# Kernel tuning notes

Hardware: AMD Instinct MI355X
Metric: run time of the kernel (lower is better)

Reference implementation:

```python
import jax, jax.numpy as jnp
import numpy as np


def setup_inputs() -> dict:
    key = jax.random.key(0)
    ks = jax.random.split(key, 6)
    L, B, S, D = 2, 32, 2048, 1024
    dec_hidden = jax.random.normal(ks[0], (L, B, D), dtype=jnp.float32)
    enc_out = jax.random.normal(ks[1], (B, S, D), dtype=jnp.float32)
    mask = jax.random.randint(ks[2], (B, S), 0, 2, dtype=jnp.int32)
    sc = 1.0 / np.sqrt(D)
    W_dec = jax.random.normal(ks[3], (D, D), dtype=jnp.float32) * sc
    W_enc = jax.random.normal(ks[4], (D, D), dtype=jnp.float32) * sc
    w_att = jax.random.normal(ks[5], (D, 1), dtype=jnp.float32) * sc
    return {
        "decoder_hidden": dec_hidden,
        "encoder_outputs": enc_out,
        "mask": mask,
        "W_dec": W_dec,
        "b_dec": jnp.zeros((D,), jnp.float32),
        "W_enc": W_enc,
        "b_enc": jnp.zeros((D,), jnp.float32),
        "w_att": w_att,
        "b_att": jnp.zeros((1,), jnp.float32),
    }


def reference(decoder_hidden, encoder_outputs, mask, W_dec, b_dec, W_enc, b_enc, w_att, b_att):
    # decoder_hidden: [L, B, Dd] -> take last layer, project to enc dim: [B, 1, De]
    dec_proj = decoder_hidden[-1] @ W_dec + b_dec            # [B, De]
    enc_proj = jnp.einsum("bse,ef->bsf", encoder_outputs, W_enc) + b_enc  # [B, S, De]
    energy = jnp.tanh(dec_proj[:, None, :] + enc_proj)        # [B, S, De]
    scores = jnp.einsum("bse,eo->bso", energy, w_att)[..., 0] + b_att[0]  # [B, S]
    scores = jnp.where(mask == 0, jnp.float32(-1e10), scores)
    attn = jax.nn.softmax(scores, axis=1)                     # [B, S]
    context = jnp.einsum("bs,bse->be", attn, encoder_outputs)[:, None, :]  # [B, 1, De]
    return context, attn
```

## Files before the change

kernel.cpp:

```cpp
#include <hip/hip_runtime.h>
#include <hip/hip_bf16.h>

constexpr int LAY = 2;
constexpr int BB  = 32;
constexpr int SS  = 2048;
constexpr int DD  = 1024;

typedef unsigned short u16;
typedef short  short8  __attribute__((ext_vector_type(8)));
typedef u16    u16x8   __attribute__((ext_vector_type(8)));
typedef float  floatx4 __attribute__((ext_vector_type(4)));

__device__ inline float bf2f(u16 u) {
    union { unsigned int i; float f; } v; v.i = ((unsigned int)u) << 16; return v.f;
}
__device__ inline u16 f2bf_rn(float f) {
    union { float f; unsigned int i; } v; v.f = f;
    unsigned int x = v.i;
    return (u16)((x + 0x7FFFu + ((x >> 16) & 1u)) >> 16);
}

__device__ __forceinline__ float fast_tanh(float x) {
    float e = __expf(x + x);
    return 1.0f - 2.0f * __builtin_amdgcn_rcpf(e + 1.0f);
}

__device__ __forceinline__ void gload_lds16(const u16* g, u16* l) {
    __builtin_amdgcn_global_load_lds(
        (const __attribute__((address_space(1))) void*)g,
        (__attribute__((address_space(3))) void*)l, 16, 0, 0);
}

__global__ __launch_bounds__(256) void convert_enc(const float* __restrict__ enc,
                                                   u16* __restrict__ encbf) {
    size_t gid = (size_t)blockIdx.x * 256 + threadIdx.x;
    #pragma unroll 4
    for (int it = 0; it < 16; ++it) {
        size_t i = (it * 524288ull + gid) * 8;
        floatx4 v0 = *reinterpret_cast<const floatx4*>(enc + i);
        floatx4 v1 = *reinterpret_cast<const floatx4*>(enc + i + 4);
        u16x8 r;
        #pragma unroll
        for (int j = 0; j < 4; ++j) { r[j] = f2bf_rn(v0[j]); r[4 + j] = f2bf_rn(v1[j]); }
        *reinterpret_cast<u16x8*>(encbf + i) = r;
    }
}

__global__ __launch_bounds__(256) void transpose_wenc(const float* __restrict__ W,
                                                      u16* __restrict__ wT) {
    int gid = blockIdx.x * 256 + threadIdx.x;
    int n = gid & 1023, c = gid >> 10;
    int k0 = c * 8;
    u16x8 r;
    #pragma unroll
    for (int j = 0; j < 8; ++j) r[j] = f2bf_rn(W[(size_t)(k0 + j) * DD + n]);
    *reinterpret_cast<u16x8*>(&wT[(size_t)n * DD + k0]) = r;
}

__global__ __launch_bounds__(256) void dec_proj_kernel(
    const float* __restrict__ dec_hidden, const float* __restrict__ W_dec,
    const float* __restrict__ b_dec, float* __restrict__ dec_proj) {
    int kc = blockIdx.x, cb = blockIdx.y, b = blockIdx.z, t = threadIdx.x;
    int col = cb * 256 + t;
    const float* h = dec_hidden + (LAY - 1) * BB * DD + b * DD + kc * 256;
    const float* Wp = W_dec + (size_t)kc * 256 * DD + col;
    float a0 = 0.f, a1 = 0.f, a2 = 0.f, a3 = 0.f;
    for (int e = 0; e < 256; e += 4) {
        a0 += h[e + 0] * Wp[(size_t)(e + 0) * DD];
        a1 += h[e + 1] * Wp[(size_t)(e + 1) * DD];
        a2 += h[e + 2] * Wp[(size_t)(e + 2) * DD];
        a3 += h[e + 3] * Wp[(size_t)(e + 3) * DD];
    }
    float v = (a0 + a1) + (a2 + a3);
    if (kc == 0) v += b_dec[col];
    atomicAdd(&dec_proj[b * DD + col], v);
}

__global__ __launch_bounds__(256) void score_gemm_bf(
    const u16* __restrict__ enc,
    const u16* __restrict__ wT,
    const float* __restrict__ dec_proj,
    const float* __restrict__ b_enc, const float* __restrict__ w_att,
    float* __restrict__ scores) {
    __shared__ u16 As[128 * 64];
    __shared__ u16 Bs[128 * 64];

    const int tid  = threadIdx.x;
    const int f    = blockIdx.x;
    const int swz  = ((f & 7) << 9) | (f >> 3);
    const int bm   = swz >> 3;
    const int bn   = swz & 7;
    const int row0 = bm * 128, col0 = bn * 128;
    const int lane = tid & 63, w = tid >> 6;
    const int wm   = w >> 1,  wn = w & 1;
    const int quad = lane >> 4, l16 = lane & 15;

    const int srow = w * 8 + (lane >> 3);
    const int scol = (((lane & 7) ^ (lane >> 3)) * 8);

    floatx4 acc[4][4];
    #pragma unroll
    for (int i = 0; i < 4; ++i)
        #pragma unroll
        for (int j = 0; j < 4; ++j)
            acc[i][j] = (floatx4){0.f, 0.f, 0.f, 0.f};

    for (int kt = 0; kt < DD / 64; ++kt) {
        const int k0 = kt * 64;
        __syncthreads();
        #pragma unroll
        for (int i = 0; i < 4; ++i) {
            gload_lds16(&enc[(size_t)(row0 + i * 32 + srow) * DD + k0 + scol],
                        &As[(i * 32 + w * 8) * 64]);
            gload_lds16(&wT [(size_t)(col0 + i * 32 + srow) * DD + k0 + scol],
                        &Bs[(i * 32 + w * 8) * 64]);
        }
        __syncthreads();
        #pragma unroll
        for (int ks = 0; ks < 2; ++ks) {
            short8 a[4], b[4];
            #pragma unroll
            for (int tm = 0; tm < 4; ++tm) {
                int r = wm * 64 + tm * 16 + l16;
                int kcs = (ks * 4 + quad) ^ (l16 & 7);
                a[tm] = *reinterpret_cast<const short8*>(&As[r * 64 + kcs * 8]);
            }
            #pragma unroll
            for (int tn = 0; tn < 4; ++tn) {
                int r = wn * 64 + tn * 16 + l16;
                int kcs = (ks * 4 + quad) ^ (l16 & 7);
                b[tn] = *reinterpret_cast<const short8*>(&Bs[r * 64 + kcs * 8]);
            }
            #pragma unroll
            for (int tm = 0; tm < 4; ++tm)
                #pragma unroll
                for (int tn = 0; tn < 4; ++tn)
                    acc[tm][tn] = __builtin_amdgcn_mfma_f32_16x16x32_bf16(
                        a[tm], b[tn], acc[tm][tn], 0, 0, 0);
        }
    }

    const int bIdx = row0 / SS;
    const float* dp = dec_proj + bIdx * DD;
    float cvec[4], wvv[4];
    #pragma unroll
    for (int tn = 0; tn < 4; ++tn) {
        int n = col0 + wn * 64 + tn * 16 + l16;
        cvec[tn] = dp[n] + b_enc[n];
        wvv[tn]  = w_att[n];
    }
    #pragma unroll
    for (int tm = 0; tm < 4; ++tm) {
        float rs0 = 0.f, rs1 = 0.f, rs2 = 0.f, rs3 = 0.f;
        #pragma unroll
        for (int tn = 0; tn < 4; ++tn) {
            rs0 += fast_tanh(acc[tm][tn][0] + cvec[tn]) * wvv[tn];
            rs1 += fast_tanh(acc[tm][tn][1] + cvec[tn]) * wvv[tn];
            rs2 += fast_tanh(acc[tm][tn][2] + cvec[tn]) * wvv[tn];
            rs3 += fast_tanh(acc[tm][tn][3] + cvec[tn]) * wvv[tn];
        }
        #pragma unroll
        for (int off = 1; off < 16; off <<= 1) {
            rs0 += __shfl_xor(rs0, off, 64);
            rs1 += __shfl_xor(rs1, off, 64);
            rs2 += __shfl_xor(rs2, off, 64);
            rs3 += __shfl_xor(rs3, off, 64);
        }
        if (l16 == 0) {
            int rbase = row0 + wm * 64 + tm * 16 + quad * 4;
            atomicAdd(&scores[rbase + 0], rs0);
            atomicAdd(&scores[rbase + 1], rs1);
            atomicAdd(&scores[rbase + 2], rs2);
            atomicAdd(&scores[rbase + 3], rs3);
        }
    }
}

__global__ __launch_bounds__(256) void softmax_kernel(
    const float* __restrict__ scores, const int* __restrict__ mask,
    float* __restrict__ attn_out) {
    int b = blockIdx.x, t = threadIdx.x;
    const float* srow = scores + b * SS;
    const int*   mrow = mask + b * SS;
    float vals[8];
    float vmax = -1e30f;
    #pragma unroll
    for (int i = 0; i < 8; ++i) {
        int s = i * 256 + t;
        float v = (mrow[s] == 0) ? -1e10f : srow[s];
        vals[i] = v;
        vmax = fmaxf(vmax, v);
    }
    #pragma unroll
    for (int off = 32; off >= 1; off >>= 1) vmax = fmaxf(vmax, __shfl_xor(vmax, off, 64));
    __shared__ float sm[4];
    if ((t & 63) == 0) sm[t >> 6] = vmax;
    __syncthreads();
    vmax = fmaxf(fmaxf(sm[0], sm[1]), fmaxf(sm[2], sm[3]));
    float sum = 0.f;
    #pragma unroll
    for (int i = 0; i < 8; ++i) { vals[i] = __expf(vals[i] - vmax); sum += vals[i]; }
    #pragma unroll
    for (int off = 32; off >= 1; off >>= 1) sum += __shfl_xor(sum, off, 64);
    __shared__ float ssum[4];
    if ((t & 63) == 0) ssum[t >> 6] = sum;
    __syncthreads();
    sum = ssum[0] + ssum[1] + ssum[2] + ssum[3];
    float inv = 1.f / sum;
    #pragma unroll
    for (int i = 0; i < 8; ++i) attn_out[b * SS + i * 256 + t] = vals[i] * inv;
}

__global__ __launch_bounds__(256) void context_bf(
    const float* __restrict__ attn, const u16* __restrict__ encbf,
    float* __restrict__ ctx) {
    int scb = blockIdx.x;
    int b   = blockIdx.y;
    int t   = threadIdx.x;
    int d   = (t & 127) * 8;
    int sh  = t >> 7;
    const float* ar  = attn + b * SS + scb * 128;
    const u16*  base = encbf + ((size_t)b * SS + scb * 128) * DD + d;
    float a[8];
    #pragma unroll
    for (int j = 0; j < 8; ++j) a[j] = 0.f;
    #pragma unroll 4
    for (int so = 0; so < 128; so += 2) {
        int s = so + sh;
        u16x8 v = *reinterpret_cast<const u16x8*>(base + (size_t)s * DD);
        float w = ar[s];
        #pragma unroll
        for (int j = 0; j < 8; ++j) a[j] += w * bf2f(v[j]);
    }
    #pragma unroll
    for (int j = 0; j < 8; ++j) atomicAdd(&ctx[b * DD + d + j], a[j]);
}

extern "C" void kernel_launch(void* const* d_in, const int* in_sizes, int n_in,
                              void* d_out, int out_size, void* d_ws, size_t ws_size,
                              hipStream_t stream) {
    const float* dec_hidden = (const float*)d_in[0];
    const float* enc        = (const float*)d_in[1];
    const int*   mask       = (const int*)d_in[2];
    const float* W_dec      = (const float*)d_in[3];
    const float* b_dec      = (const float*)d_in[4];
    const float* W_enc      = (const float*)d_in[5];
    const float* b_enc      = (const float*)d_in[6];
    const float* w_att      = (const float*)d_in[7];

    float* out = (float*)d_out;
    float* ws  = (float*)d_ws;
    float* dec_proj = ws;
    float* scores   = ws + 32768;
    u16*   wT       = (u16*)(ws + 98304);
    u16*   encbf    = (u16*)(ws + 622592);
    float* attn     = out + 32768;

    hipMemsetAsync(ws, 0, 98304 * sizeof(float), stream);
    hipMemsetAsync(out, 0, 32768 * sizeof(float), stream);

    convert_enc<<<2048, 256, 0, stream>>>(enc, encbf);
    transpose_wenc<<<512, 256, 0, stream>>>(W_enc, wT);
    dec_proj_kernel<<<dim3(4, 4, 32), 256, 0, stream>>>(dec_hidden, W_dec, b_dec, dec_proj);
    score_gemm_bf<<<4096, 256, 0, stream>>>(encbf, wT, dec_proj, b_enc, w_att, scores);
    softmax_kernel<<<32, 256, 0, stream>>>(scores, mask, attn);
    context_bf<<<dim3(16, 32), 256, 0, stream>>>(attn, encbf, out);
}
```

Measured before the change: 697.8 us.

## Enlarge score GEMM tiles to 256x256 with double-buffered LDS pipelining

The bf16 score GEMM moves from 128x128 tiles with 4 waves to 256x256 tiles with 8 waves, each wave holding an 8x4 MFMA accumulator block. LDS is double-buffered, so the next K-slice loads are issued while MFMAs run on the current buffer, with split A/B staging and s_setprio around the MFMA bursts. The aim is more data reuse per loaded byte and overlap of global-to-LDS copies with compute. In exchange it uses 128KB of LDS per block and more accumulator registers, which caps occupancy, and the grid shrinks to 1024 blocks.

```diff
diff --git a/kernel.cpp b/kernel.cpp
--- a/kernel.cpp
+++ b/kernel.cpp
@@ -76,69 +76,47 @@
     atomicAdd(&dec_proj[b * DD + col], v);
 }
 
-__global__ __launch_bounds__(256) void score_gemm_bf(
+__global__ __launch_bounds__(512, 2) void score_gemm_bf(
     const u16* __restrict__ enc,
     const u16* __restrict__ wT,
     const float* __restrict__ dec_proj,
     const float* __restrict__ b_enc, const float* __restrict__ w_att,
     float* __restrict__ scores) {
-    __shared__ u16 As[128 * 64];
-    __shared__ u16 Bs[128 * 64];
+    __shared__ u16 As[2][256 * 64];
+    __shared__ u16 Bs[2][256 * 64];
 
     const int tid  = threadIdx.x;
     const int f    = blockIdx.x;
-    const int swz  = ((f & 7) << 9) | (f >> 3);
-    const int bm   = swz >> 3;
-    const int bn   = swz & 7;
-    const int row0 = bm * 128, col0 = bn * 128;
+    const int swz  = ((f & 7) << 7) | (f >> 3);
+    const int bm   = swz >> 2;
+    const int bn   = swz & 3;
+    const int row0 = bm * 256, col0 = bn * 256;
     const int lane = tid & 63, w = tid >> 6;
-    const int wm   = w >> 1,  wn = w & 1;
+    const int wm   = w >> 2,  wn = w & 3;
     const int quad = lane >> 4, l16 = lane & 15;
 
     const int srow = w * 8 + (lane >> 3);
     const int scol = (((lane & 7) ^ (lane >> 3)) * 8);
 
-    floatx4 acc[4][4];
-    #pragma unroll
-    for (int i = 0; i < 4; ++i)
+    auto stageA = [&](int buf, int k0) {
+        #pragma unroll
+        for (int i = 0; i < 4; ++i)
+            gload_lds16(&enc[(size_t)(row0 + i * 64 + srow) * DD + k0 + scol],
+                        &As[buf][(i * 64 + w * 8) * 64]);
+    };
+    auto stageB = [&](int buf, int k0) {
+        #pragma unroll
+        for (int i = 0; i < 4; ++i)
+            gload_lds16(&wT[(size_t)(col0 + i * 64 + srow) * DD + k0 + scol],
+                        &Bs[buf][(i * 64 + w * 8) * 64]);
+    };
+
+    floatx4 acc[8][4];
+    #pragma unroll
+    for (int i = 0; i < 8; ++i)
         #pragma unroll
         for (int j = 0; j < 4; ++j)
             acc[i][j] = (floatx4){0.f, 0.f, 0.f, 0.f};
-
-    for (int kt = 0; kt < DD / 64; ++kt) {
-        const int k0 = kt * 64;
-        __syncthreads();
-        #pragma unroll
-        for (int i = 0; i < 4; ++i) {
-            gload_lds16(&enc[(size_t)(row0 + i * 32 + srow) * DD + k0 + scol],
-                        &As[(i * 32 + w * 8) * 64]);
-            gload_lds16(&wT [(size_t)(col0 + i * 32 + srow) * DD + k0 + scol],
-                        &Bs[(i * 32 + w * 8) * 64]);
-        }
-        __syncthreads();
-        #pragma unroll
-        for (int ks = 0; ks < 2; ++ks) {
-            short8 a[4], b[4];
-            #pragma unroll
-            for (int tm = 0; tm < 4; ++tm) {
-                int r = wm * 64 + tm * 16 + l16;
-                int kcs = (ks * 4 + quad) ^ (l16 & 7);
-                a[tm] = *reinterpret_cast<const short8*>(&As[r * 64 + kcs * 8]);
-            }
-            #pragma unroll
-            for (int tn = 0; tn < 4; ++tn) {
-                int r = wn * 64 + tn * 16 + l16;
-                int kcs = (ks * 4 + quad) ^ (l16 & 7);
-                b[tn] = *reinterpret_cast<const short8*>(&Bs[r * 64 + kcs * 8]);
-            }
-            #pragma unroll
-            for (int tm = 0; tm < 4; ++tm)
-                #pragma unroll
-                for (int tn = 0; tn < 4; ++tn)
-                    acc[tm][tn] = __builtin_amdgcn_mfma_f32_16x16x32_bf16(
-                        a[tm], b[tn], acc[tm][tn], 0, 0, 0);
-        }
-    }
 
     const int bIdx = row0 / SS;
     const float* dp = dec_proj + bIdx * DD;
@@ -149,8 +127,54 @@
         cvec[tn] = dp[n] + b_enc[n];
         wvv[tn]  = w_att[n];
     }
-    #pragma unroll
-    for (int tm = 0; tm < 4; ++tm) {
+
+    auto phase = [&](int buf, int ks) {
+        short8 a[8], b[4];
+        const int kcs = (ks * 4 + quad) ^ (l16 & 7);
+        #pragma unroll
+        for (int m = 0; m < 8; ++m) {
+            int r = wm * 128 + m * 16 + l16;
+            a[m] = *reinterpret_cast<const short8*>(&As[buf][r * 64 + kcs * 8]);
+        }
+        #pragma unroll
+        for (int n = 0; n < 4; ++n) {
+            int r = wn * 64 + n * 16 + l16;
+            b[n] = *reinterpret_cast<const short8*>(&Bs[buf][r * 64 + kcs * 8]);
+        }
+        __builtin_amdgcn_s_setprio(1);
+        #pragma unroll
+        for (int m = 0; m < 8; ++m)
+            #pragma unroll
+            for (int n = 0; n < 4; ++n)
+                acc[m][n] = __builtin_amdgcn_mfma_f32_16x16x32_bf16(
+                    a[m], b[n], acc[m][n], 0, 0, 0);
+        __builtin_amdgcn_s_setprio(0);
+    };
+
+    #define MID_BAR  do { __builtin_amdgcn_s_barrier(); \
+                          __builtin_amdgcn_sched_barrier(0); } while (0)
+
+    stageA(0, 0); stageB(0, 0);
+    __syncthreads();
+
+    for (int kt = 0; kt < 16; kt += 2) {
+        if (kt + 1 < 16) stageA(1, (kt + 1) * 64);
+        phase(0, 0);
+        MID_BAR;
+        if (kt + 1 < 16) stageB(1, (kt + 1) * 64);
+        phase(0, 1);
+        __syncthreads();
+        if (kt + 2 < 16) stageA(0, (kt + 2) * 64);
+        phase(1, 0);
+        MID_BAR;
+        if (kt + 2 < 16) stageB(0, (kt + 2) * 64);
+        phase(1, 1);
+        __syncthreads();
+    }
+    #undef MID_BAR
+
+    #pragma unroll
+    for (int tm = 0; tm < 8; ++tm) {
         float rs0 = 0.f, rs1 = 0.f, rs2 = 0.f, rs3 = 0.f;
         #pragma unroll
         for (int tn = 0; tn < 4; ++tn) {
@@ -167,7 +191,7 @@
             rs3 += __shfl_xor(rs3, off, 64);
         }
         if (l16 == 0) {
-            int rbase = row0 + wm * 64 + tm * 16 + quad * 4;
+            int rbase = row0 + wm * 128 + tm * 16 + quad * 4;
             atomicAdd(&scores[rbase + 0], rs0);
             atomicAdd(&scores[rbase + 1], rs1);
             atomicAdd(&scores[rbase + 2], rs2);
@@ -262,7 +286,7 @@
     convert_enc<<<2048, 256, 0, stream>>>(enc, encbf);
     transpose_wenc<<<512, 256, 0, stream>>>(W_enc, wT);
     dec_proj_kernel<<<dim3(4, 4, 32), 256, 0, stream>>>(dec_hidden, W_dec, b_dec, dec_proj);
-    score_gemm_bf<<<4096, 256, 0, stream>>>(encbf, wT, dec_proj, b_enc, w_att, scores);
+    score_gemm_bf<<<1024, 512, 0, stream>>>(encbf, wT, dec_proj, b_enc, w_att, scores);
     softmax_kernel<<<32, 256, 0, stream>>>(scores, mask, attn);
     context_bf<<<dim3(16, 32), 256, 0, stream>>>(attn, encbf, out);
 }
```

New measurement: 665.1 us. -4.7%, faster.

## Retile score GEMM to 64x256 with register-direct W fragments and double-buffered A

Applied to the files above, without the earlier changes.

W_enc is now pre-packed into an MFMA-fragment layout, so the score GEMM reads B fragments straight from global memory into registers instead of staging them through LDS. The A tile shrinks to 64 rows and is double-buffered in LDS, while each block covers 256 output columns with four waves, and occupancy is hinted at 4 blocks per CU. The decoder projection now computes all 32 batch rows per block from shared memory so each weight element is read once, and the context kernel grid is doubled for more parallelism. The trade-off is more global and L2 traffic for B fragments each k-step and more atomics in dec_proj, in exchange for less LDS pressure, one fewer barrier per iteration, and overlap of A loads with compute.

```diff
diff --git a/kernel.cpp b/kernel.cpp
--- a/kernel.cpp
+++ b/kernel.cpp
@@ -47,56 +47,70 @@
 }
 
 __global__ __launch_bounds__(256) void transpose_wenc(const float* __restrict__ W,
-                                                      u16* __restrict__ wT) {
+                                                      u16* __restrict__ wt2) {
     int gid = blockIdx.x * 256 + threadIdx.x;
     int n = gid & 1023, c = gid >> 10;
-    int k0 = c * 8;
     u16x8 r;
     #pragma unroll
-    for (int j = 0; j < 8; ++j) r[j] = f2bf_rn(W[(size_t)(k0 + j) * DD + n]);
-    *reinterpret_cast<u16x8*>(&wT[(size_t)n * DD + k0]) = r;
+    for (int j = 0; j < 8; ++j) r[j] = f2bf_rn(W[(size_t)(c * 8 + j) * DD + n]);
+    *reinterpret_cast<u16x8*>(&wt2[((size_t)c * DD + n) * 8]) = r;
 }
 
 __global__ __launch_bounds__(256) void dec_proj_kernel(
     const float* __restrict__ dec_hidden, const float* __restrict__ W_dec,
     const float* __restrict__ b_dec, float* __restrict__ dec_proj) {
-    int kc = blockIdx.x, cb = blockIdx.y, b = blockIdx.z, t = threadIdx.x;
+    int kc = blockIdx.x, cb = blockIdx.y, t = threadIdx.x;
     int col = cb * 256 + t;
-    const float* h = dec_hidden + (LAY - 1) * BB * DD + b * DD + kc * 256;
-    const float* Wp = W_dec + (size_t)kc * 256 * DD + col;
-    float a0 = 0.f, a1 = 0.f, a2 = 0.f, a3 = 0.f;
-    for (int e = 0; e < 256; e += 4) {
-        a0 += h[e + 0] * Wp[(size_t)(e + 0) * DD];
-        a1 += h[e + 1] * Wp[(size_t)(e + 1) * DD];
-        a2 += h[e + 2] * Wp[(size_t)(e + 2) * DD];
-        a3 += h[e + 3] * Wp[(size_t)(e + 3) * DD];
-    }
-    float v = (a0 + a1) + (a2 + a3);
-    if (kc == 0) v += b_dec[col];
-    atomicAdd(&dec_proj[b * DD + col], v);
-}
-
-__global__ __launch_bounds__(256) void score_gemm_bf(
+    __shared__ float sh[32][64];
+    const float* hbase = dec_hidden + (LAY - 1) * BB * DD + kc * 64;
+    #pragma unroll
+    for (int j = 0; j < 8; ++j) {
+        int idx = t + j * 256;
+        int b = idx >> 6, e = idx & 63;
+        sh[b][e] = hbase[(size_t)b * DD + e];
+    }
+    __syncthreads();
+    float acc[32];
+    #pragma unroll
+    for (int b = 0; b < 32; ++b) acc[b] = 0.f;
+    const float* Wp = W_dec + (size_t)kc * 64 * DD + col;
+    for (int e = 0; e < 64; ++e) {
+        float wv = Wp[(size_t)e * DD];
+        #pragma unroll
+        for (int b = 0; b < 32; ++b) acc[b] += sh[b][e] * wv;
+    }
+    float bd = (kc == 0) ? b_dec[col] : 0.f;
+    #pragma unroll
+    for (int b = 0; b < 32; ++b) atomicAdd(&dec_proj[b * DD + col], acc[b] + bd);
+}
+
+__global__ __launch_bounds__(256, 4) void score_gemm_bf(
     const u16* __restrict__ enc,
-    const u16* __restrict__ wT,
+    const u16* __restrict__ wt2,
     const float* __restrict__ dec_proj,
     const float* __restrict__ b_enc, const float* __restrict__ w_att,
     float* __restrict__ scores) {
-    __shared__ u16 As[128 * 64];
-    __shared__ u16 Bs[128 * 64];
+    __shared__ u16 As[2][64 * 64];
 
     const int tid  = threadIdx.x;
     const int f    = blockIdx.x;
     const int swz  = ((f & 7) << 9) | (f >> 3);
-    const int bm   = swz >> 3;
-    const int bn   = swz & 7;
-    const int row0 = bm * 128, col0 = bn * 128;
+    const int bm   = swz >> 2;
+    const int bn   = swz & 3;
+    const int row0 = bm * 64, col0 = bn * 256;
     const int lane = tid & 63, w = tid >> 6;
-    const int wm   = w >> 1,  wn = w & 1;
     const int quad = lane >> 4, l16 = lane & 15;
 
-    const int srow = w * 8 + (lane >> 3);
+    const int srow = lane >> 3;
     const int scol = (((lane & 7) ^ (lane >> 3)) * 8);
+
+    auto stage = [&](int buf, int kt) {
+        const int k0 = kt * 64;
+        #pragma unroll
+        for (int i = 0; i < 2; ++i)
+            gload_lds16(&enc[(size_t)(row0 + w * 16 + i * 8 + srow) * DD + k0 + scol],
+                        &As[buf][(w * 16 + i * 8) * 64]);
+    };
 
     floatx4 acc[4][4];
     #pragma unroll
@@ -105,39 +119,54 @@
         for (int j = 0; j < 4; ++j)
             acc[i][j] = (floatx4){0.f, 0.f, 0.f, 0.f};
 
-    for (int kt = 0; kt < DD / 64; ++kt) {
-        const int k0 = kt * 64;
+    const u16* bbase = wt2 + ((size_t)quad * DD + col0 + w * 64 + l16) * 8;
+
+    stage(0, 0);
+    __syncthreads();
+
+    int buf = 0;
+    for (int kt = 0; kt < 16; ++kt) {
+        short8 b0[4], b1[4];
+        const u16* bk = bbase + (size_t)kt * 8 * DD * 8;
+        #pragma unroll
+        for (int n = 0; n < 4; ++n)
+            b0[n] = *reinterpret_cast<const short8*>(bk + (size_t)n * 16 * 8);
+        #pragma unroll
+        for (int n = 0; n < 4; ++n)
+            b1[n] = *reinterpret_cast<const short8*>(bk + (size_t)4 * DD * 8 + (size_t)n * 16 * 8);
+        if (kt + 1 < 16) stage(buf ^ 1, kt + 1);
+        {
+            short8 a[4];
+            #pragma unroll
+            for (int m = 0; m < 4; ++m) {
+                int r = m * 16 + l16;
+                int kcs = quad ^ (l16 & 7);
+                a[m] = *reinterpret_cast<const short8*>(&As[buf][r * 64 + kcs * 8]);
+            }
+            #pragma unroll
+            for (int m = 0; m < 4; ++m)
+                #pragma unroll
+                for (int n = 0; n < 4; ++n)
+                    acc[m][n] = __builtin_amdgcn_mfma_f32_16x16x32_bf16(
+                        a[m], b0[n], acc[m][n], 0, 0, 0);
+        }
+        {
+            short8 a[4];
+            #pragma unroll
+            for (int m = 0; m < 4; ++m) {
+                int r = m * 16 + l16;
+                int kcs = (4 + quad) ^ (l16 & 7);
+                a[m] = *reinterpret_cast<const short8*>(&As[buf][r * 64 + kcs * 8]);
+            }
+            #pragma unroll
+            for (int m = 0; m < 4; ++m)
+                #pragma unroll
+                for (int n = 0; n < 4; ++n)
+                    acc[m][n] = __builtin_amdgcn_mfma_f32_16x16x32_bf16(
+                        a[m], b1[n], acc[m][n], 0, 0, 0);
+        }
         __syncthreads();
-        #pragma unroll
-        for (int i = 0; i < 4; ++i) {
-            gload_lds16(&enc[(size_t)(row0 + i * 32 + srow) * DD + k0 + scol],
-                        &As[(i * 32 + w * 8) * 64]);
-            gload_lds16(&wT [(size_t)(col0 + i * 32 + srow) * DD + k0 + scol],
-                        &Bs[(i * 32 + w * 8) * 64]);
-        }
-        __syncthreads();
-        #pragma unroll
-        for (int ks = 0; ks < 2; ++ks) {
-            short8 a[4], b[4];
-            #pragma unroll
-            for (int tm = 0; tm < 4; ++tm) {
-                int r = wm * 64 + tm * 16 + l16;
-                int kcs = (ks * 4 + quad) ^ (l16 & 7);
-                a[tm] = *reinterpret_cast<const short8*>(&As[r * 64 + kcs * 8]);
-            }
-            #pragma unroll
-            for (int tn = 0; tn < 4; ++tn) {
-                int r = wn * 64 + tn * 16 + l16;
-                int kcs = (ks * 4 + quad) ^ (l16 & 7);
-                b[tn] = *reinterpret_cast<const short8*>(&Bs[r * 64 + kcs * 8]);
-            }
-            #pragma unroll
-            for (int tm = 0; tm < 4; ++tm)
-                #pragma unroll
-                for (int tn = 0; tn < 4; ++tn)
-                    acc[tm][tn] = __builtin_amdgcn_mfma_f32_16x16x32_bf16(
-                        a[tm], b[tn], acc[tm][tn], 0, 0, 0);
-        }
+        buf ^= 1;
     }
 
     const int bIdx = row0 / SS;
@@ -145,7 +174,7 @@
     float cvec[4], wvv[4];
     #pragma unroll
     for (int tn = 0; tn < 4; ++tn) {
-        int n = col0 + wn * 64 + tn * 16 + l16;
+        int n = col0 + w * 64 + tn * 16 + l16;
         cvec[tn] = dp[n] + b_enc[n];
         wvv[tn]  = w_att[n];
     }
@@ -167,7 +196,7 @@
             rs3 += __shfl_xor(rs3, off, 64);
         }
         if (l16 == 0) {
-            int rbase = row0 + wm * 64 + tm * 16 + quad * 4;
+            int rbase = row0 + tm * 16 + quad * 4;
             atomicAdd(&scores[rbase + 0], rs0);
             atomicAdd(&scores[rbase + 1], rs1);
             atomicAdd(&scores[rbase + 2], rs2);
@@ -219,13 +248,13 @@
     int t   = threadIdx.x;
     int d   = (t & 127) * 8;
     int sh  = t >> 7;
-    const float* ar  = attn + b * SS + scb * 128;
-    const u16*  base = encbf + ((size_t)b * SS + scb * 128) * DD + d;
+    const float* ar  = attn + b * SS + scb * 64;
+    const u16*  base = encbf + ((size_t)b * SS + scb * 64) * DD + d;
     float a[8];
     #pragma unroll
     for (int j = 0; j < 8; ++j) a[j] = 0.f;
     #pragma unroll 4
-    for (int so = 0; so < 128; so += 2) {
+    for (int so = 0; so < 64; so += 2) {
         int s = so + sh;
         u16x8 v = *reinterpret_cast<const u16x8*>(base + (size_t)s * DD);
         float w = ar[s];
@@ -252,7 +281,7 @@
     float* ws  = (float*)d_ws;
     float* dec_proj = ws;
     float* scores   = ws + 32768;
-    u16*   wT       = (u16*)(ws + 98304);
+    u16*   wt2      = (u16*)(ws + 98304);
     u16*   encbf    = (u16*)(ws + 622592);
     float* attn     = out + 32768;
 
@@ -260,9 +289,9 @@
     hipMemsetAsync(out, 0, 32768 * sizeof(float), stream);
 
     convert_enc<<<2048, 256, 0, stream>>>(enc, encbf);
-    transpose_wenc<<<512, 256, 0, stream>>>(W_enc, wT);
-    dec_proj_kernel<<<dim3(4, 4, 32), 256, 0, stream>>>(dec_hidden, W_dec, b_dec, dec_proj);
-    score_gemm_bf<<<4096, 256, 0, stream>>>(encbf, wT, dec_proj, b_enc, w_att, scores);
+    transpose_wenc<<<512, 256, 0, stream>>>(W_enc, wt2);
+    dec_proj_kernel<<<dim3(16, 4), 256, 0, stream>>>(dec_hidden, W_dec, b_dec, dec_proj);
+    score_gemm_bf<<<4096, 256, 0, stream>>>(encbf, wt2, dec_proj, b_enc, w_att, scores);
     softmax_kernel<<<32, 256, 0, stream>>>(scores, mask, attn);
-    context_bf<<<dim3(16, 32), 256, 0, stream>>>(attn, encbf, out);
-}
+    context_bf<<<dim3(32, 32), 256, 0, stream>>>(attn, encbf, out);
+}
```

Measured after the change: 681.2 us. -2.4%, faster.
